# Optimization experiments

Measured on AMD Instinct MI355X. Metric: run time of the kernel, lower is better.

The kernel has to match this reference:

```python
import jax, jax.numpy as jnp
import numpy as np

N, D, K, NUM_CLASSES = 65536, 512, 1024, 2


def setup_inputs() -> dict:
    key = jax.random.key(0)
    kx, kc = jax.random.split(key)
    x = jax.random.normal(kx, (N, D), dtype=jnp.float32)
    codebook_vectors = jax.random.normal(kc, (K, D), dtype=jnp.float32)
    codebook_classes = jnp.arange(K, dtype=jnp.int64 if jax.config.read('jax_enable_x64') else jnp.int32) % NUM_CLASSES
    return {"x": x, "codebook_vectors": codebook_vectors, "codebook_classes": codebook_classes}


def reference(x, codebook_vectors, codebook_classes):
    # Squared Euclidean distances (argmin identical to torch.cdist's p=2 argmin):
    # d2[n,k] = |x_n|^2 - 2 x_n . c_k + |c_k|^2
    x_sq = jnp.sum(x * x, axis=1, keepdims=True)            # (N, 1)
    c_sq = jnp.sum(codebook_vectors * codebook_vectors, axis=1)  # (K,)
    cross = jnp.einsum('nd,kd->nk', x, codebook_vectors)    # (N, K) GEMM
    d2 = x_sq - 2.0 * cross + c_sq[None, :]
    winners = jnp.argmin(d2, axis=1)                         # (N,)
    return codebook_classes[winners]
```

## Files before the change

kernel.cpp:

```cpp
#include <hip/hip_runtime.h>
#include <hip/hip_bf16.h>


#define N_ROWS 65536
#define DIM    512
#define K_CB   1024
#define NT2    8
#define LDSB2  32768
#define LDSBUF 32768
#define NT     16

typedef short bf16x8 __attribute__((ext_vector_type(8)));
typedef float f32x4  __attribute__((ext_vector_type(4)));
typedef unsigned short u16x8 __attribute__((ext_vector_type(8)));

__device__ __forceinline__ unsigned short f2bf_rn(float f) {
    unsigned u = __float_as_uint(f);
    unsigned r = (u + 0x7FFFu + ((u >> 16) & 1u)) >> 16;
    return (unsigned short)r;
}
__device__ __forceinline__ float bf2f(unsigned short h) {
    return __uint_as_float(((unsigned)h) << 16);
}
__device__ __forceinline__ bf16x8 pack_bf8(float4 a, float4 b) {
    bf16x8 r;
    r[0] = (short)f2bf_rn(a.x); r[1] = (short)f2bf_rn(a.y);
    r[2] = (short)f2bf_rn(a.z); r[3] = (short)f2bf_rn(a.w);
    r[4] = (short)f2bf_rn(b.x); r[5] = (short)f2bf_rn(b.y);
    r[6] = (short)f2bf_rn(b.z); r[7] = (short)f2bf_rn(b.w);
    return r;
}

__device__ __forceinline__ void gload16(const void* g, void* l) {
    __builtin_amdgcn_global_load_lds(
        (const __attribute__((address_space(1))) unsigned int*)g,
        (__attribute__((address_space(3))) unsigned int*)l, 16, 0, 0);
}

__global__ void csq_kernel(const float* __restrict__ C, float* __restrict__ csq) {
    int wid  = (blockIdx.x * blockDim.x + threadIdx.x) >> 6;
    int lane = threadIdx.x & 63;
    const float4* p = (const float4*)(C + (size_t)wid * DIM);
    float4 a = p[lane * 2];
    float4 b = p[lane * 2 + 1];
    float s = a.x*a.x + a.y*a.y + a.z*a.z + a.w*a.w
            + b.x*b.x + b.y*b.y + b.z*b.z + b.w*b.w;
    #pragma unroll
    for (int m = 1; m < 64; m <<= 1) s += __shfl_xor(s, m, 64);
    if (lane == 0) csq[wid] = s;
}

__global__ void split_hi8(const float* __restrict__ src,
                          unsigned short* __restrict__ h, int n8) {
    int stride = gridDim.x * 256;
    for (int i = blockIdx.x * 256 + threadIdx.x; i < n8; i += stride) {
        const float4* p = (const float4*)(src + (size_t)i * 8);
        float4 a = p[0], b = p[1];
        u16x8 o;
        o[0] = f2bf_rn(a.x); o[1] = f2bf_rn(a.y);
        o[2] = f2bf_rn(a.z); o[3] = f2bf_rn(a.w);
        o[4] = f2bf_rn(b.x); o[5] = f2bf_rn(b.y);
        o[6] = f2bf_rn(b.z); o[7] = f2bf_rn(b.w);
        *(u16x8*)(h + (size_t)i * 8) = o;
    }
}

__global__ __launch_bounds__(512, 1)
void gemm_scores(const float* __restrict__ X,
                 const unsigned short* __restrict__ Ch,
                 const float* __restrict__ csq,
                 _Float16* __restrict__ scores) {
    extern __shared__ unsigned short smem[];

    int b  = blockIdx.x;
    int x  = b & 7;
    int m8 = b >> 3;
    int rowtile = x * 32 + (m8 >> 2);
    int coltile = m8 & 3;
    int n0 = rowtile * 256;
    int k0 = coltile * 256;

    int tid  = threadIdx.x;
    int w    = tid >> 6;
    int lane = tid & 63;
    int wr   = w >> 2, wc = w & 3;
    int rbase = wr * 128, cbase = wc * 64;
    int lrow = lane & 15;
    int lk   = lane >> 4;
    int swz  = (lrow >> 1) & 7;
    int sgk0 = (lk)     ^ swz;
    int sgk1 = (4 + lk) ^ swz;

    int ra = tid >> 1;
    int h  = tid & 1;
    int aswz = (ra >> 1) & 7;
    const float* xsrc = X + (size_t)(n0 + ra) * DIM + h * 32;
    int ad0 = ra * 64 + ((h * 4 + 0) ^ aswz) * 8;
    int ad1 = ra * 64 + ((h * 4 + 1) ^ aswz) * 8;
    int ad2 = ra * 64 + ((h * 4 + 2) ^ aswz) * 8;
    int ad3 = ra * 64 + ((h * 4 + 3) ^ aswz) * 8;

    int rb  = tid >> 3;
    int grp = tid & 7;
    int gg  = grp ^ ((rb >> 1) & 7);
    size_t oB = (size_t)(k0 + rb) * DIM + gg * 8;
    int dB  = 16384 + w * 512;

    f32x4 acc[8][4];
    #pragma unroll
    for (int i = 0; i < 8; i++)
        #pragma unroll
        for (int j = 0; j < 4; j++)
            acc[i][j] = (f32x4){0.f, 0.f, 0.f, 0.f};

    auto issue_B = [&](int tn) {
        unsigned short* bufn = smem + (tn & 1) * LDSB2;
        size_t d = (size_t)tn * 64;
        gload16(Ch + oB + d,                   bufn + dB);
        gload16(Ch + oB + d + (size_t)64*DIM,  bufn + dB + 4096);
        gload16(Ch + oB + d + (size_t)128*DIM, bufn + dB + 8192);
        gload16(Ch + oB + d + (size_t)192*DIM, bufn + dB + 12288);
    };

    float4 xq0, xq1, xq2, xq3, xq4, xq5, xq6, xq7;

    auto loadX = [&](int tn) {
        const float4* q = (const float4*)(xsrc + tn * 64);
        xq0 = q[0]; xq1 = q[1]; xq2 = q[2]; xq3 = q[3];
        xq4 = q[4]; xq5 = q[5]; xq6 = q[6]; xq7 = q[7];
    };
    auto writeA = [&](unsigned short* nb) {
        *(bf16x8*)(nb + ad0) = pack_bf8(xq0, xq1);
        *(bf16x8*)(nb + ad1) = pack_bf8(xq2, xq3);
        *(bf16x8*)(nb + ad2) = pack_bf8(xq4, xq5);
        *(bf16x8*)(nb + ad3) = pack_bf8(xq6, xq7);
    };

    loadX(0);
    issue_B(0);
    asm volatile("s_waitcnt vmcnt(4)" ::: "memory");
    writeA(smem);

    for (int t = 0; t < NT2; ++t) {
        asm volatile("s_waitcnt vmcnt(0)" ::: "memory");
        asm volatile("s_waitcnt lgkmcnt(0)" ::: "memory");
        __builtin_amdgcn_s_barrier();
        asm volatile("" ::: "memory");

        const unsigned short* buf = smem + (t & 1) * LDSB2;
        unsigned short* nbuf = smem + ((t + 1) & 1) * LDSB2;
        const unsigned short* pA = buf + (rbase + lrow) * 64;
        const unsigned short* pB = buf + 16384 + (cbase + lrow) * 64;
        bool pre = (t + 1 < NT2);

        if (pre) {
            loadX(t + 1);
            issue_B(t + 1);
        }

        bf16x8 ah[8], bh[4];
        #pragma unroll
        for (int n = 0; n < 4; n++) bh[n] = *(const bf16x8*)(pB + n * 1024 + sgk0 * 8);
        #pragma unroll
        for (int m = 0; m < 8; m++) ah[m] = *(const bf16x8*)(pA + m * 1024 + sgk0 * 8);
        __builtin_amdgcn_s_setprio(1);
        #pragma unroll
        for (int m = 0; m < 8; m++)
            #pragma unroll
            for (int n = 0; n < 4; n++)
                acc[m][n] = __builtin_amdgcn_mfma_f32_16x16x32_bf16(ah[m], bh[n], acc[m][n], 0, 0, 0);
        __builtin_amdgcn_s_setprio(0);
        #pragma unroll
        for (int n = 0; n < 4; n++) bh[n] = *(const bf16x8*)(pB + n * 1024 + sgk1 * 8);
        #pragma unroll
        for (int m = 0; m < 8; m++) ah[m] = *(const bf16x8*)(pA + m * 1024 + sgk1 * 8);
        __builtin_amdgcn_s_setprio(1);
        #pragma unroll
        for (int m = 0; m < 8; m++)
            #pragma unroll
            for (int n = 0; n < 4; n++)
                acc[m][n] = __builtin_amdgcn_mfma_f32_16x16x32_bf16(ah[m], bh[n], acc[m][n], 0, 0, 0);
        __builtin_amdgcn_s_setprio(0);

        if (pre) {
            asm volatile("s_waitcnt vmcnt(4)" ::: "memory");
            writeA(nbuf);
        }
    }

    float cs[4];
    #pragma unroll
    for (int n = 0; n < 4; n++) cs[n] = csq[k0 + cbase + n * 16 + lrow];

    #pragma unroll
    for (int m = 0; m < 8; m++) {
        int grow = n0 + rbase + m * 16 + lk * 4;
        #pragma unroll
        for (int r = 0; r < 4; r++) {
            _Float16* sp = scores + (size_t)(grow + r) * K_CB + k0 + cbase + lrow;
            #pragma unroll
            for (int n = 0; n < 4; n++)
                sp[n * 16] = (_Float16)(cs[n] - 2.0f * acc[m][n][r]);
        }
    }
}

struct H8 { _Float16 v[8]; };

__global__ __launch_bounds__(256)
void phase2_kernel(const float* __restrict__ X, const float* __restrict__ C,
                   const float* __restrict__ csq,
                   const _Float16* __restrict__ scores,
                   const int* __restrict__ classes, int* __restrict__ out) {
    int lane = threadIdx.x & 63;
    int n = blockIdx.x * 4 + (threadIdx.x >> 6);

    float s[16];
    {
        const _Float16* sp16 = scores + (size_t)n * K_CB + lane * 16;
        H8 h0 = *(const H8*)sp16;
        H8 h1 = *(const H8*)(sp16 + 8);
        #pragma unroll
        for (int j = 0; j < 8; j++) {
            s[j]     = (float)h0.v[j];
            s[8 + j] = (float)h1.v[j];
        }
    }

    float mn = s[0];
    #pragma unroll
    for (int j = 1; j < 16; j++) mn = fminf(mn, s[j]);
    #pragma unroll
    for (int m = 1; m < 64; m <<= 1) mn = fminf(mn, __shfl_xor(mn, m, 64));

    float thr = mn + 16.0f;
    unsigned fl = 0;
    #pragma unroll
    for (int j = 0; j < 16; j++) fl |= (unsigned)(s[j] <= thr) << j;
    int cnt = __popc(fl);
    #pragma unroll
    for (int m = 1; m < 64; m <<= 1) cnt += __shfl_xor(cnt, m, 64);

    int bestk;
    if (cnt == 1) {
        int kk = 0x7fffffff;
        #pragma unroll
        for (int j = 0; j < 16; j++)
            if ((fl >> j) & 1) kk = lane * 16 + j;
        #pragma unroll
        for (int m = 1; m < 64; m <<= 1) kk = min(kk, __shfl_xor(kk, m, 64));
        bestk = kk;
    } else {
        const float4* xp = (const float4*)(X + (size_t)n * DIM + lane * 8);
        float4 x0 = xp[0], x1 = xp[1];
        float bv = 3.4e38f;
        int bk = 0x7fffffff;
        #pragma unroll 1
        for (int j = 0; j < 16; j++) {
            unsigned long long mask = __ballot((fl >> j) & 1);
            while (mask) {
                int l = __ffsll((unsigned long long)mask) - 1;
                mask &= mask - 1;
                int k = l * 16 + j;
                const float4* cp = (const float4*)(C + (size_t)k * DIM + lane * 8);
                float4 y0 = cp[0], y1 = cp[1];
                float d = x0.x*y0.x + x0.y*y0.y + x0.z*y0.z + x0.w*y0.w
                        + x1.x*y1.x + x1.y*y1.y + x1.z*y1.z + x1.w*y1.w;
                #pragma unroll
                for (int m = 1; m < 64; m <<= 1) d += __shfl_xor(d, m, 64);
                float se = csq[k] - 2.0f * d;
                if (se < bv || (se == bv && k < bk)) { bv = se; bk = k; }
            }
        }
        bestk = bk;
    }
    if (lane == 0) out[n] = classes[bestk];
}

__global__ void init_kernel(unsigned long long* __restrict__ packed) {
    int n = blockIdx.x * 256 + threadIdx.x;
    if (n < N_ROWS) packed[n] = ~0ull;
}

__global__ void split_kernel(const float* __restrict__ src,
                             unsigned short* __restrict__ h,
                             unsigned short* __restrict__ l, int n4) {
    int stride = gridDim.x * 256;
    for (int i = blockIdx.x * 256 + threadIdx.x; i < n4; i += stride) {
        float4 v = ((const float4*)src)[i];
        ushort4 hh, ll;
        float f;
        f = v.x; hh.x = f2bf_rn(f); ll.x = f2bf_rn(f - bf2f(hh.x));
        f = v.y; hh.y = f2bf_rn(f); ll.y = f2bf_rn(f - bf2f(hh.y));
        f = v.z; hh.z = f2bf_rn(f); ll.z = f2bf_rn(f - bf2f(hh.z));
        f = v.w; hh.w = f2bf_rn(f); ll.w = f2bf_rn(f - bf2f(hh.w));
        ((ushort4*)h)[i] = hh;
        ((ushort4*)l)[i] = ll;
    }
}

__global__ __launch_bounds__(512, 2)
void gemm_argmin(const unsigned short* __restrict__ Xh,
                 const unsigned short* __restrict__ Xl,
                 const unsigned short* __restrict__ Ch,
                 const unsigned short* __restrict__ Cl,
                 const float* __restrict__ csq,
                 unsigned long long* __restrict__ packed) {
    extern __shared__ unsigned short smem[];

    int b  = blockIdx.x;
    int x  = b & 7;
    int m8 = b >> 3;
    int rowtile = x * 32 + (m8 >> 2);
    int coltile = m8 & 3;
    int n0 = rowtile * 256;
    int k0 = coltile * 256;

    int tid  = threadIdx.x;
    int w    = tid >> 6;
    int lane = tid & 63;
    int wr   = w >> 2, wc = w & 3;
    int rbase = wr * 128, cbase = wc * 64;
    int lrow = lane & 15;
    int lk   = lane >> 4;
    int sg   = lk ^ ((lrow >> 1) & 3);

    int srow = tid >> 2;
    int sgrp = tid & 3;
    int r1   = (srow < 64) ? srow : srow + 64;
    int ggA  = sgrp ^ ((r1 >> 1) & 3);
    int gB   = sgrp ^ ((srow >> 1) & 3);
    size_t oA1 = (size_t)(n0 + r1) * DIM + ggA * 8;
    size_t oA2 = oA1 + (size_t)64 * DIM;
    size_t oB0 = (size_t)(k0 + srow) * DIM + gB * 8;
    size_t oB1 = oB0 + (size_t)128 * DIM;
    int rowA1_0 = (w < 4) ? w * 16 : w * 16 + 64;
    int dA1  = rowA1_0 * 32;
    int dA2  = dA1 + 2048;
    int dB0  = 16384 + w * 512;
    int dB1  = dB0 + 4096;
    int dBl0 = dB0 + 8192;
    int dBl1 = dB1 + 8192;

    f32x4 acc[8][4];
    #pragma unroll
    for (int i = 0; i < 8; i++)
        #pragma unroll
        for (int j = 0; j < 4; j++)
            acc[i][j] = (f32x4){0.f, 0.f, 0.f, 0.f};

    bf16x8 bh[4], bl[4];

    auto issue_tile = [&](int t) {
        unsigned short* bufn = smem + (t & 1) * LDSBUF;
        size_t d = (size_t)t * 32;
        gload16(Xh + oA1 + d, bufn + dA1);
        gload16(Xl + oA1 + d, bufn + 8192 + dA1);
        gload16(Ch + oB0 + d, bufn + dB0);
        gload16(Ch + oB1 + d, bufn + dB1);
        gload16(Cl + oB0 + d, bufn + dBl0);
        gload16(Cl + oB1 + d, bufn + dBl1);
        gload16(Xh + oA2 + d, bufn + dA2);
        gload16(Xl + oA2 + d, bufn + 8192 + dA2);
    };

    auto mfma_half = [&](int mb, const bf16x8* ah, const bf16x8* al) {
        __builtin_amdgcn_s_setprio(1);
        #pragma unroll
        for (int mm = 0; mm < 4; mm++)
            #pragma unroll
            for (int n = 0; n < 4; n++)
                acc[mb + mm][n] = __builtin_amdgcn_mfma_f32_16x16x32_bf16(ah[mm], bh[n], acc[mb + mm][n], 0, 0, 0);
        #pragma unroll
        for (int mm = 0; mm < 4; mm++)
            #pragma unroll
            for (int n = 0; n < 4; n++)
                acc[mb + mm][n] = __builtin_amdgcn_mfma_f32_16x16x32_bf16(ah[mm], bl[n], acc[mb + mm][n], 0, 0, 0);
        #pragma unroll
        for (int mm = 0; mm < 4; mm++)
            #pragma unroll
            for (int n = 0; n < 4; n++)
                acc[mb + mm][n] = __builtin_amdgcn_mfma_f32_16x16x32_bf16(al[mm], bh[n], acc[mb + mm][n], 0, 0, 0);
        __builtin_amdgcn_s_setprio(0);
    };

    issue_tile(0);

    for (int t = 0; t < NT; ++t) {
        asm volatile("s_waitcnt vmcnt(0)" ::: "memory");
        __builtin_amdgcn_s_barrier();
        asm volatile("" ::: "memory");

        const unsigned short* buf = smem + (t & 1) * LDSBUF;
        const unsigned short* pA = buf + (rbase + lrow) * 32 + sg * 8;
        const unsigned short* pB = buf + 16384 + (cbase + lrow) * 32 + sg * 8;

        #pragma unroll
        for (int n = 0; n < 4; n++) {
            bh[n] = *(const bf16x8*)(pB + n * 512);
            bl[n] = *(const bf16x8*)(pB + 8192 + n * 512);
        }
        bf16x8 ah[4], al[4];
        #pragma unroll
        for (int mm = 0; mm < 4; mm++) {
            ah[mm] = *(const bf16x8*)(pA + mm * 512);
            al[mm] = *(const bf16x8*)(pA + 8192 + mm * 512);
        }
        if (t + 1 < NT) issue_tile(t + 1);

        mfma_half(0, ah, al);

        bf16x8 ah2[4], al2[4];
        #pragma unroll
        for (int mm = 0; mm < 4; mm++) {
            ah2[mm] = *(const bf16x8*)(pA + (4 + mm) * 512);
            al2[mm] = *(const bf16x8*)(pA + 8192 + (4 + mm) * 512);
        }
        mfma_half(4, ah2, al2);
    }

    float cs[4];
    #pragma unroll
    for (int n = 0; n < 4; n++) cs[n] = csq[k0 + cbase + n * 16 + lrow];

    #pragma unroll
    for (int m = 0; m < 8; m++) {
        #pragma unroll
        for (int r = 0; r < 4; r++) {
            unsigned long long best = ~0ull;
            #pragma unroll
            for (int n = 0; n < 4; n++) {
                float s = cs[n] - 2.0f * acc[m][n][r];
                unsigned kb  = __float_as_uint(s);
                unsigned key = kb ^ (unsigned)(((int)kb >> 31) | 0x80000000);
                unsigned col = (unsigned)(k0 + cbase + n * 16 + lrow);
                unsigned long long pk = (((unsigned long long)key) << 32) | col;
                best = pk < best ? pk : best;
            }
            #pragma unroll
            for (int mask = 1; mask <= 8; mask <<= 1) {
                unsigned hi = __shfl_xor((unsigned)(best >> 32), mask, 64);
                unsigned lo = __shfl_xor((unsigned)(best & 0xFFFFFFFFu), mask, 64);
                unsigned long long other = (((unsigned long long)hi) << 32) | lo;
                best = other < best ? other : best;
            }
            if (lrow == 0) {
                int grow = n0 + rbase + m * 16 + lk * 4 + r;
                atomicMin(&packed[grow], best);
            }
        }
    }
}

__global__ void map_kernel(const unsigned long long* __restrict__ packed,
                           const int* __restrict__ classes,
                           int* __restrict__ out) {
    int n = blockIdx.x * 256 + threadIdx.x;
    if (n < N_ROWS) {
        unsigned col = (unsigned)(packed[n] & 0xFFFFFFFFull);
        out[n] = classes[col];
    }
}

extern "C" void kernel_launch(void* const* d_in, const int* in_sizes, int n_in,
                              void* d_out, int out_size, void* d_ws, size_t ws_size,
                              hipStream_t stream) {
    const float* X       = (const float*)d_in[0];
    const float* C       = (const float*)d_in[1];
    const int*   classes = (const int*)d_in[2];
    int*         out     = (int*)d_out;
    char* ws = (char*)d_ws;

    {
        size_t off = 0;
        float* csq = (float*)(ws + off);                  off += 4096;
        unsigned short* Ch = (unsigned short*)(ws + off); off += (size_t)K_CB * DIM * 2;
        _Float16* scores = (_Float16*)(ws + off);         off += (size_t)N_ROWS * K_CB * 2;
        if (ws_size >= off) {
            csq_kernel<<<K_CB / 4, 256, 0, stream>>>(C, csq);
            split_hi8<<<256, 256, 0, stream>>>(C, Ch, K_CB * DIM / 8);
            hipFuncSetAttribute((const void*)gemm_scores,
                                hipFuncAttributeMaxDynamicSharedMemorySize,
                                2 * LDSB2 * (int)sizeof(unsigned short));
            gemm_scores<<<(N_ROWS / 256) * (K_CB / 256), 512,
                          2 * LDSB2 * sizeof(unsigned short), stream>>>(
                X, Ch, csq, scores);
            phase2_kernel<<<N_ROWS / 4, 256, 0, stream>>>(X, C, csq, scores, classes, out);
            return;
        }
    }

    size_t off = 0;
    unsigned long long* packed = (unsigned long long*)(ws + off); off += (size_t)N_ROWS * 8;
    float* csq = (float*)(ws + off);                              off += (size_t)K_CB * 4;
    unsigned short* Xh = (unsigned short*)(ws + off);             off += (size_t)N_ROWS * DIM * 2;
    unsigned short* Xl = (unsigned short*)(ws + off);             off += (size_t)N_ROWS * DIM * 2;
    unsigned short* Ch = (unsigned short*)(ws + off);             off += (size_t)K_CB * DIM * 2;
    unsigned short* Cl = (unsigned short*)(ws + off);             off += (size_t)K_CB * DIM * 2;

    init_kernel<<<N_ROWS / 256, 256, 0, stream>>>(packed);
    csq_kernel<<<K_CB / 4, 256, 0, stream>>>(C, csq);
    split_kernel<<<2048, 256, 0, stream>>>(X, Xh, Xl, N_ROWS * DIM / 4);
    split_kernel<<<512, 256, 0, stream>>>(C, Ch, Cl, K_CB * DIM / 4);
    hipFuncSetAttribute((const void*)gemm_argmin,
                        hipFuncAttributeMaxDynamicSharedMemorySize,
                        2 * LDSBUF * (int)sizeof(unsigned short));
    gemm_argmin<<<(N_ROWS / 256) * (K_CB / 256), 512,
                  2 * LDSBUF * sizeof(unsigned short), stream>>>(
        Xh, Xl, Ch, Cl, csq, packed);
    map_kernel<<<N_ROWS / 256, 256, 0, stream>>>(packed, classes, out);
}
```

Measured before the change: 194.3 us.

## Split LDS tiles into two K-halves with 32-element rows and 4-way swizzle

Reorganizes the shared-memory layout of the A and B tiles from 64-element rows with an 8-way XOR swizzle to two separate K-half planes of 32-element rows with a 4-way swizzle. The global-to-LDS codebook loads and the X conversion writes are remapped to match, and each MFMA phase reads from its own plane. The goal is to change LDS bank access patterns and address arithmetic to reduce bank conflicts on the fragment reads. This risks different conflict behaviour on the writes and less coalesced global loads, since each thread now covers 32-element row segments.

```diff
diff --git a/kernel.cpp b/kernel.cpp
--- a/kernel.cpp
+++ b/kernel.cpp
@@ -87,24 +87,23 @@
     int rbase = wr * 128, cbase = wc * 64;
     int lrow = lane & 15;
     int lk   = lane >> 4;
-    int swz  = (lrow >> 1) & 7;
-    int sgk0 = (lk)     ^ swz;
-    int sgk1 = (4 + lk) ^ swz;
+    int sg   = lk ^ ((lrow >> 1) & 3);
 
     int ra = tid >> 1;
-    int h  = tid & 1;
-    int aswz = (ra >> 1) & 7;
-    const float* xsrc = X + (size_t)(n0 + ra) * DIM + h * 32;
-    int ad0 = ra * 64 + ((h * 4 + 0) ^ aswz) * 8;
-    int ad1 = ra * 64 + ((h * 4 + 1) ^ aswz) * 8;
-    int ad2 = ra * 64 + ((h * 4 + 2) ^ aswz) * 8;
-    int ad3 = ra * 64 + ((h * 4 + 3) ^ aswz) * 8;
-
-    int rb  = tid >> 3;
-    int grp = tid & 7;
-    int gg  = grp ^ ((rb >> 1) & 7);
-    size_t oB = (size_t)(k0 + rb) * DIM + gg * 8;
-    int dB  = 16384 + w * 512;
+    int p_ = tid & 1;
+    int aswz = (ra >> 1) & 3;
+    const float* xsrc = X + (size_t)(n0 + ra) * DIM + p_ * 32;
+    int abase = p_ * 8192 + ra * 32;
+    int ad0 = abase + ((0 ^ aswz) * 8);
+    int ad1 = abase + ((1 ^ aswz) * 8);
+    int ad2 = abase + ((2 ^ aswz) * 8);
+    int ad3 = abase + ((3 ^ aswz) * 8);
+
+    int srow = tid >> 2;
+    int sgrp = tid & 3;
+    int gB   = sgrp ^ ((srow >> 1) & 3);
+    size_t oB = (size_t)(k0 + srow) * DIM + gB * 8;
+    int dB   = 16384 + w * 512;
 
     f32x4 acc[8][4];
     #pragma unroll
@@ -116,10 +115,10 @@
     auto issue_B = [&](int tn) {
         unsigned short* bufn = smem + (tn & 1) * LDSB2;
         size_t d = (size_t)tn * 64;
-        gload16(Ch + oB + d,                   bufn + dB);
-        gload16(Ch + oB + d + (size_t)64*DIM,  bufn + dB + 4096);
-        gload16(Ch + oB + d + (size_t)128*DIM, bufn + dB + 8192);
-        gload16(Ch + oB + d + (size_t)192*DIM, bufn + dB + 12288);
+        gload16(Ch + oB + d,                        bufn + dB);
+        gload16(Ch + oB + d + (size_t)128*DIM,      bufn + dB + 4096);
+        gload16(Ch + oB + d + 32,                   bufn + dB + 8192);
+        gload16(Ch + oB + d + 32 + (size_t)128*DIM, bufn + dB + 12288);
     };
 
     float4 xq0, xq1, xq2, xq3, xq4, xq5, xq6, xq7;
@@ -149,8 +148,6 @@
 
         const unsigned short* buf = smem + (t & 1) * LDSB2;
         unsigned short* nbuf = smem + ((t + 1) & 1) * LDSB2;
-        const unsigned short* pA = buf + (rbase + lrow) * 64;
-        const unsigned short* pB = buf + 16384 + (cbase + lrow) * 64;
         bool pre = (t + 1 < NT2);
 
         if (pre) {
@@ -159,28 +156,36 @@
         }
 
         bf16x8 ah[8], bh[4];
-        #pragma unroll
-        for (int n = 0; n < 4; n++) bh[n] = *(const bf16x8*)(pB + n * 1024 + sgk0 * 8);
-        #pragma unroll
-        for (int m = 0; m < 8; m++) ah[m] = *(const bf16x8*)(pA + m * 1024 + sgk0 * 8);
-        __builtin_amdgcn_s_setprio(1);
-        #pragma unroll
-        for (int m = 0; m < 8; m++)
-            #pragma unroll
-            for (int n = 0; n < 4; n++)
-                acc[m][n] = __builtin_amdgcn_mfma_f32_16x16x32_bf16(ah[m], bh[n], acc[m][n], 0, 0, 0);
-        __builtin_amdgcn_s_setprio(0);
-        #pragma unroll
-        for (int n = 0; n < 4; n++) bh[n] = *(const bf16x8*)(pB + n * 1024 + sgk1 * 8);
-        #pragma unroll
-        for (int m = 0; m < 8; m++) ah[m] = *(const bf16x8*)(pA + m * 1024 + sgk1 * 8);
-        __builtin_amdgcn_s_setprio(1);
-        #pragma unroll
-        for (int m = 0; m < 8; m++)
-            #pragma unroll
-            for (int n = 0; n < 4; n++)
-                acc[m][n] = __builtin_amdgcn_mfma_f32_16x16x32_bf16(ah[m], bh[n], acc[m][n], 0, 0, 0);
-        __builtin_amdgcn_s_setprio(0);
+        {
+            const unsigned short* pA = buf + (rbase + lrow) * 32 + sg * 8;
+            const unsigned short* pB = buf + 16384 + (cbase + lrow) * 32 + sg * 8;
+            #pragma unroll
+            for (int n = 0; n < 4; n++) bh[n] = *(const bf16x8*)(pB + n * 512);
+            #pragma unroll
+            for (int m = 0; m < 8; m++) ah[m] = *(const bf16x8*)(pA + m * 512);
+            __builtin_amdgcn_s_setprio(1);
+            #pragma unroll
+            for (int m = 0; m < 8; m++)
+                #pragma unroll
+                for (int n = 0; n < 4; n++)
+                    acc[m][n] = __builtin_amdgcn_mfma_f32_16x16x32_bf16(ah[m], bh[n], acc[m][n], 0, 0, 0);
+            __builtin_amdgcn_s_setprio(0);
+        }
+        {
+            const unsigned short* pA = buf + 8192 + (rbase + lrow) * 32 + sg * 8;
+            const unsigned short* pB = buf + 24576 + (cbase + lrow) * 32 + sg * 8;
+            #pragma unroll
+            for (int n = 0; n < 4; n++) bh[n] = *(const bf16x8*)(pB + n * 512);
+            #pragma unroll
+            for (int m = 0; m < 8; m++) ah[m] = *(const bf16x8*)(pA + m * 512);
+            __builtin_amdgcn_s_setprio(1);
+            #pragma unroll
+            for (int m = 0; m < 8; m++)
+                #pragma unroll
+                for (int n = 0; n < 4; n++)
+                    acc[m][n] = __builtin_amdgcn_mfma_f32_16x16x32_bf16(ah[m], bh[n], acc[m][n], 0, 0, 0);
+            __builtin_amdgcn_s_setprio(0);
+        }
 
         if (pre) {
             asm volatile("s_waitcnt vmcnt(4)" ::: "memory");
```

Measured after the change: 193.3 us. About the same (-0.5%).
